# Kernel tuning notes

Hardware: AMD Instinct MI355X
Metric: run time of the kernel (lower is better)

The kernel has to match this reference:

```python
import jax, jax.numpy as jnp
import numpy as np

POOL = 4      # pool_size
SR = 2        # sampling_ratio (fixed; torchvision adaptive default approximated)
C_IN = 1024
C1, C2 = 256, 128
OUT_DIM = 2048


def setup_inputs() -> dict:
    key = jax.random.key(0)
    ks = jax.random.split(key, 10)
    B, C, H, W = 8, C_IN, 64, 64
    N = 64
    x = jax.random.normal(ks[0], (B, C, H, W), dtype=jnp.float32)
    # boxes in image pixel coords (image is H*16 = 1024 px)
    img = 1024.0
    x1 = jax.random.uniform(ks[1], (B, N), minval=0.0, maxval=img - 260.0)
    y1 = jax.random.uniform(ks[2], (B, N), minval=0.0, maxval=img - 260.0)
    bw = jax.random.uniform(ks[3], (B, N), minval=32.0, maxval=256.0)
    bh = jax.random.uniform(ks[4], (B, N), minval=32.0, maxval=256.0)
    boxes = jnp.stack([x1, y1, x1 + bw, y1 + bh], axis=-1)  # [B,N,4]
    scale = jnp.float32(1.0 / 16.0)
    # detector params
    w1 = jax.random.normal(ks[5], (C1, C_IN), dtype=jnp.float32) / np.sqrt(C_IN)
    b1 = jnp.zeros((C1,), dtype=jnp.float32)
    w2 = jax.random.normal(ks[6], (C2, C1), dtype=jnp.float32) / np.sqrt(C1)
    b2 = jnp.zeros((C2,), dtype=jnp.float32)
    wl = jax.random.normal(ks[7], (OUT_DIM, C2 * POOL * POOL), dtype=jnp.float32) / np.sqrt(C2 * POOL * POOL)
    bl = jnp.zeros((OUT_DIM,), dtype=jnp.float32)
    return {"x": x, "boxes": boxes, "scale": scale,
            "w1": w1, "b1": b1, "w2": w2, "b2": b2, "wl": wl, "bl": bl}


def _axis_coords(start, size, H):
    # start,size: [R]; returns coords [R, POOL*SR], valid mask, int low/high, lerp wts
    bin_sz = size / POOL                       # [R]
    j = jnp.arange(POOL * SR, dtype=jnp.float32)
    off = jnp.floor(j / SR) + ((j % SR) + 0.5) / SR   # [P]
    c = start[:, None] + off[None, :] * bin_sz[:, None]  # [R,P]
    valid = (c >= -1.0) & (c <= H)
    c = jnp.clip(c, 0.0, H - 1.0)
    lo = jnp.floor(c).astype(jnp.int32)
    lo = jnp.minimum(lo, H - 1)
    hi = jnp.minimum(lo + 1, H - 1)
    frac = c - lo.astype(c.dtype)
    return valid, lo, hi, frac


def _roi_align(feat, boxes, scale):
    # feat: [B,C,H,W], boxes: [B,N,4] -> pooled [B*N, C, POOL, POOL]
    B, C, H, W = feat.shape
    N = boxes.shape[1]
    R = B * N
    bx = (boxes.reshape(R, 4) * scale)
    x1, y1, x2, y2 = bx[:, 0], bx[:, 1], bx[:, 2], bx[:, 3]
    rw = jnp.maximum(x2 - x1, 1.0)
    rh = jnp.maximum(y2 - y1, 1.0)
    vy, y_lo, y_hi, ly = _axis_coords(y1, rh, H)   # [R,P]
    vx, x_lo, x_hi, lx = _axis_coords(x1, rw, W)
    hy, hx = 1.0 - ly, 1.0 - lx
    bidx = jnp.repeat(jnp.arange(B, dtype=jnp.int32), N)  # [R]
    b = bidx[:, None, None]
    # gather 4 corners -> [R,P,P,C]
    v00 = feat[b, :, y_lo[:, :, None], x_lo[:, None, :]]
    v01 = feat[b, :, y_lo[:, :, None], x_hi[:, None, :]]
    v10 = feat[b, :, y_hi[:, :, None], x_lo[:, None, :]]
    v11 = feat[b, :, y_hi[:, :, None], x_hi[:, None, :]]
    w00 = (hy[:, :, None] * hx[:, None, :])[..., None]
    w01 = (hy[:, :, None] * lx[:, None, :])[..., None]
    w10 = (ly[:, :, None] * hx[:, None, :])[..., None]
    w11 = (ly[:, :, None] * lx[:, None, :])[..., None]
    val = v00 * w00 + v01 * w01 + v10 * w10 + v11 * w11
    mask = (vy[:, :, None] & vx[:, None, :])[..., None]
    val = jnp.where(mask, val, 0.0)            # [R,P,P,C]
    val = val.reshape(R, POOL, SR, POOL, SR, C).mean(axis=(2, 4))  # [R,POOL,POOL,C]
    return jnp.transpose(val, (0, 3, 1, 2))    # [R,C,POOL,POOL]


def reference(x, boxes, scale, w1, b1, w2, b2, wl, bl):
    pooled = _roi_align(x, boxes, scale)                  # [R,C,4,4]
    h = jax.nn.elu(jnp.einsum('rchw,oc->rohw', pooled, w1) + b1[None, :, None, None])
    h = jax.nn.elu(jnp.einsum('rchw,oc->rohw', h, w2) + b2[None, :, None, None])
    h = h.reshape(h.shape[0], -1)                         # [R, 128*16], torch Flatten order
    out = jax.nn.elu(h @ wl.T + bl)                       # [R, 2048]
    return out
```

## Files before the change

### kernel.cpp

```cpp
#include <hip/hip_runtime.h>
#include <math.h>

#define C_INK   1024
#define C1D     256
#define C2D     128
#define OUTD    2048
#define R_ROI   512
#define MPIX    32768

#define NSIDE   128

typedef _Float16 half8 __attribute__((ext_vector_type(8)));
typedef float    f32x4 __attribute__((ext_vector_type(4)));

__device__ __forceinline__ unsigned int pack2h(float a, float b) {
    union { _Float16 h[2]; unsigned int u; } p;
    p.h[0] = (_Float16)a; p.h[1] = (_Float16)b;
    return p.u;
}
__device__ __forceinline__ float eluf(float v) { return v > 0.f ? v : expf(v) - 1.f; }

template<int RC>
__device__ __forceinline__ half8* ldsq(_Float16* base, int row, int ch) {
    return reinterpret_cast<half8*>(base) + row * RC + (ch ^ (row & 7));
}

__global__ __launch_bounds__(512, 4) void conv1x1_f16(
    const float* __restrict__ x, const float* __restrict__ w1,
    const float* __restrict__ w2, const float* __restrict__ wl,
    _Float16* __restrict__ w2h, _Float16* __restrict__ wlh,
    _Float16* __restrict__ z)
{
    const int bid = blockIdx.x;
    const int tid = threadIdx.x;

    if (bid < NSIDE) {
        constexpr int NF4_W2 = (C2D * C1D) / 4;
        constexpr int NF4    = NF4_W2 + (OUTD * OUTD) / 4;
        for (int i = bid * 512 + tid; i < NF4; i += NSIDE * 512) {
            const float* s; _Float16* d; int e;
            if (i < NF4_W2) { s = w2; d = w2h; e = i * 4; }
            else            { s = wl; d = wlh; e = (i - NF4_W2) * 4; }
            const float4 v = *reinterpret_cast<const float4*>(s + e);
            uint2 u; u.x = pack2h(v.x, v.y); u.y = pack2h(v.z, v.w);
            *reinterpret_cast<uint2*>(d + e) = u;
        }
        return;
    }

    __shared__ __align__(16) _Float16 As[64 * 64];
    __shared__ __align__(16) _Float16 Bs[256 * 64];

    const int lane = tid & 63;
    const int wave = tid >> 6;
    const int m0   = (bid - NSIDE) * 64;
    const int b    = m0 >> 12;
    const int p0   = m0 & 4095;

    const int bc  = tid & 7;
    const int br0 = tid >> 3;

    float ar[8];
    half8 brg[4];
    f32x4 acc[4][2];
    #pragma unroll
    for (int i = 0; i < 4; ++i)
        #pragma unroll
        for (int j = 0; j < 2; ++j) acc[i][j] = (f32x4){0.f, 0.f, 0.f, 0.f};

    const float* xbase = x + (size_t)b * C_INK * 4096 + p0 + lane;

    auto LOADT = [&](int k0) {
        const float* xk = xbase + (size_t)(k0 + wave * 8) * 4096;
        #pragma unroll
        for (int j = 0; j < 8; ++j) ar[j] = xk[(size_t)j * 4096];
        #pragma unroll
        for (int i = 0; i < 4; ++i) {
            const float* wp = &w1[(size_t)(br0 + i * 64) * C_INK + k0 + bc * 8];
            const float4 v0 = *reinterpret_cast<const float4*>(wp);
            const float4 v1 = *reinterpret_cast<const float4*>(wp + 4);
            union { half8 h; unsigned int u[4]; } pk;
            pk.u[0] = pack2h(v0.x, v0.y); pk.u[1] = pack2h(v0.z, v0.w);
            pk.u[2] = pack2h(v1.x, v1.y); pk.u[3] = pack2h(v1.z, v1.w);
            brg[i] = pk.h;
        }
    };
    auto WRITET = [&]() {
        union { half8 h; unsigned int u[4]; } pk;
        #pragma unroll
        for (int j = 0; j < 4; ++j) pk.u[j] = pack2h(ar[2 * j], ar[2 * j + 1]);
        *ldsq<8>(As, lane, wave) = pk.h;
        #pragma unroll
        for (int i = 0; i < 4; ++i) *ldsq<8>(Bs, br0 + i * 64, bc) = brg[i];
    };
    auto COMPUTET = [&]() {
        #pragma unroll
        for (int kk = 0; kk < 2; ++kk) {
            const int ch = kk * 4 + (lane >> 4);
            half8 af[4], bf[2];
            #pragma unroll
            for (int mi = 0; mi < 4; ++mi) af[mi] = *ldsq<8>(As, mi * 16 + (lane & 15), ch);
            #pragma unroll
            for (int ni = 0; ni < 2; ++ni) bf[ni] = *ldsq<8>(Bs, wave * 32 + ni * 16 + (lane & 15), ch);
            #pragma unroll
            for (int mi = 0; mi < 4; ++mi)
                #pragma unroll
                for (int ni = 0; ni < 2; ++ni)
                    acc[mi][ni] = __builtin_amdgcn_mfma_f32_16x16x32_f16(bf[ni], af[mi], acc[mi][ni], 0, 0, 0);
        }
    };

    LOADT(0); WRITET(); __syncthreads();
    for (int t = 0; t < 15; ++t) {
        LOADT((t + 1) * 64);
        COMPUTET();
        __syncthreads();
        WRITET();
        __syncthreads();
    }
    COMPUTET();

    _Float16* zp = z + (size_t)m0 * C1D;
    #pragma unroll
    for (int mi = 0; mi < 4; ++mi) {
        const int pixel = mi * 16 + (lane & 15);
        #pragma unroll
        for (int ni = 0; ni < 2; ++ni) {
            const int oc0 = wave * 32 + ni * 16 + (lane >> 4) * 4;
            uint2 u;
            u.x = pack2h(acc[mi][ni][0], acc[mi][ni][1]);
            u.y = pack2h(acc[mi][ni][2], acc[mi][ni][3]);
            *reinterpret_cast<uint2*>(&zp[(size_t)pixel * C1D + oc0]) = u;
        }
    }
}

__global__ __launch_bounds__(512) void roi_gemm2_f16(
    const _Float16* __restrict__ z, const float* __restrict__ boxes,
    const float* __restrict__ scale_p, const float* __restrict__ b1v,
    const _Float16* __restrict__ w2h, const float* __restrict__ b2v,
    _Float16* __restrict__ h2)
{
    __shared__ __align__(16) _Float16 H1s[16 * 256];
    __shared__ int   s_off[64][4];
    __shared__ float s_w[64][4];

    const int bid  = blockIdx.x;
    const int r    = (bid & 7) * 64 + (bid >> 3);
    const int tid  = threadIdx.x;
    const int lane = tid & 63;
    const int wv   = tid >> 6;

    half8 bfr[8];
    {
        const _Float16* wp = w2h + (size_t)(wv * 16 + (lane & 15)) * C1D + (lane >> 4) * 8;
        #pragma unroll
        for (int ks = 0; ks < 8; ++ks)
            bfr[ks] = *reinterpret_cast<const half8*>(wp + ks * 32);
    }

    if (tid < 64) {
        const float sc = scale_p[0];
        const float x1 = boxes[r * 4 + 0] * sc, y1 = boxes[r * 4 + 1] * sc;
        const float x2 = boxes[r * 4 + 2] * sc, y2 = boxes[r * 4 + 3] * sc;
        const float rw = fmaxf(x2 - x1, 1.f), rh = fmaxf(y2 - y1, 1.f);
        const int jy = tid >> 3, jx = tid & 7;

        float offy = (float)(jy >> 1) + (float)(jy & 1) * 0.5f + 0.25f;
        float cy = y1 + offy * rh * 0.25f;
        const bool vy = (cy >= -1.f) && (cy <= 64.f);
        cy = fminf(fmaxf(cy, 0.f), 63.f);
        int ylo = (int)cy; if (ylo > 63) ylo = 63;
        int yhi = ylo + 1; if (yhi > 63) yhi = 63;
        const float ly = cy - (float)ylo, hy = 1.f - ly;

        float offx = (float)(jx >> 1) + (float)(jx & 1) * 0.5f + 0.25f;
        float cx = x1 + offx * rw * 0.25f;
        const bool vx = (cx >= -1.f) && (cx <= 64.f);
        cx = fminf(fmaxf(cx, 0.f), 63.f);
        int xlo = (int)cx; if (xlo > 63) xlo = 63;
        int xhi = xlo + 1; if (xhi > 63) xhi = 63;
        const float lx = cx - (float)xlo, hx = 1.f - lx;

        const float wm = (vy && vx) ? 0.25f : 0.f;
        s_w[tid][0] = hy * hx * wm;
        s_w[tid][1] = hy * lx * wm;
        s_w[tid][2] = ly * hx * wm;
        s_w[tid][3] = ly * lx * wm;
        s_off[tid][0] = (ylo * 64 + xlo) * C1D;
        s_off[tid][1] = (ylo * 64 + xhi) * C1D;
        s_off[tid][2] = (yhi * 64 + xlo) * C1D;
        s_off[tid][3] = (yhi * 64 + xhi) * C1D;
    }
    __syncthreads();

    {
        const int ch8  = tid & 31;
        const int cell = tid >> 5;
        const _Float16* zb = z + (size_t)(r >> 6) * 4096 * C1D + ch8 * 8;

        float accv[8];
        #pragma unroll
        for (int e = 0; e < 8; ++e) accv[e] = 0.f;

        const int py = cell >> 2, px = cell & 3;
        #pragma unroll
        for (int u = 0; u < 4; ++u) {
            const int s = (py * 2 + (u >> 1)) * 8 + px * 2 + (u & 1);
            #pragma unroll
            for (int k = 0; k < 4; ++k) {
                const half8 v = *reinterpret_cast<const half8*>(zb + s_off[s][k]);
                const float w = s_w[s][k];
                #pragma unroll
                for (int e = 0; e < 8; ++e) accv[e] += (float)v[e] * w;
            }
        }

        const float4 b0 = *reinterpret_cast<const float4*>(&b1v[ch8 * 8]);
        const float4 b4 = *reinterpret_cast<const float4*>(&b1v[ch8 * 8 + 4]);
        half8 o;
        o[0] = (_Float16)eluf(accv[0] + b0.x); o[1] = (_Float16)eluf(accv[1] + b0.y);
        o[2] = (_Float16)eluf(accv[2] + b0.z); o[3] = (_Float16)eluf(accv[3] + b0.w);
        o[4] = (_Float16)eluf(accv[4] + b4.x); o[5] = (_Float16)eluf(accv[5] + b4.y);
        o[6] = (_Float16)eluf(accv[6] + b4.z); o[7] = (_Float16)eluf(accv[7] + b4.w);
        *ldsq<32>(H1s, cell, ch8) = o;
    }
    __syncthreads();

    f32x4 oa = (f32x4){0.f, 0.f, 0.f, 0.f};
    #pragma unroll
    for (int ks = 0; ks < 8; ++ks) {
        const int ch = ks * 4 + (lane >> 4);
        const half8 af = *ldsq<32>(H1s, lane & 15, ch);
        oa = __builtin_amdgcn_mfma_f32_16x16x32_f16(af, bfr[ks], oa, 0, 0, 0);
    }

    {
        const int o  = wv * 16 + (lane & 15);
        const int p0 = (lane >> 4) * 4;
        const float bv = b2v[o];
        uint2 u;
        u.x = pack2h(eluf(oa[0] + bv), eluf(oa[1] + bv));
        u.y = pack2h(eluf(oa[2] + bv), eluf(oa[3] + bv));
        *reinterpret_cast<uint2*>(&h2[(size_t)r * 2048 + o * 16 + p0]) = u;
    }
}

__global__ __launch_bounds__(512) void gemm_nt_out(
    const _Float16* __restrict__ A, const _Float16* __restrict__ W,
    const float* __restrict__ bias, float* __restrict__ Cout)
{
    constexpr int K = OUTD, N = OUTD;
    __shared__ __align__(16) _Float16 As[64 * 128];
    __shared__ __align__(16) _Float16 Bs[64 * 128];

    const int bid  = blockIdx.x;
    const int m0   = (bid >> 5) * 64;
    const int n0   = (bid & 31) * 64;

    const int tid  = threadIdx.x;
    const int lane = tid & 63;
    const int wave = tid >> 6;
    const int wr   = wave >> 2, wc = wave & 3;
    const int c    = tid & 7;
    const int r0   = tid >> 3;

    half8 arg[2], brg[2];
    f32x4 acc[2];
    acc[0] = (f32x4){0.f, 0.f, 0.f, 0.f};
    acc[1] = (f32x4){0.f, 0.f, 0.f, 0.f};

    auto LOADT = [&](int k0) {
        const _Float16* ap = &A[(size_t)(m0 + r0) * K + k0 + c * 16];
        arg[0] = *reinterpret_cast<const half8*>(ap);
        arg[1] = *reinterpret_cast<const half8*>(ap + 8);
        const _Float16* wp = &W[(size_t)(n0 + r0) * K + k0 + c * 16];
        brg[0] = *reinterpret_cast<const half8*>(wp);
        brg[1] = *reinterpret_cast<const half8*>(wp + 8);
    };
    auto WRITET = [&]() {
        *ldsq<16>(As, r0, 2 * c)     = arg[0];
        *ldsq<16>(As, r0, 2 * c + 1) = arg[1];
        *ldsq<16>(Bs, r0, 2 * c)     = brg[0];
        *ldsq<16>(Bs, r0, 2 * c + 1) = brg[1];
    };
    auto COMPUTET = [&]() {
        #pragma unroll
        for (int kk = 0; kk < 4; ++kk) {
            const int ch = kk * 4 + (lane >> 4);
            half8 af[2], bf;
            af[0] = *ldsq<16>(As, wr * 32 + (lane & 15), ch);
            af[1] = *ldsq<16>(As, wr * 32 + 16 + (lane & 15), ch);
            bf    = *ldsq<16>(Bs, wc * 16 + (lane & 15), ch);
            acc[0] = __builtin_amdgcn_mfma_f32_16x16x32_f16(bf, af[0], acc[0], 0, 0, 0);
            acc[1] = __builtin_amdgcn_mfma_f32_16x16x32_f16(bf, af[1], acc[1], 0, 0, 0);
        }
    };

    constexpr int nt = K / 128;
    LOADT(0); WRITET(); __syncthreads();
    for (int t = 0; t < nt - 1; ++t) {
        LOADT((t + 1) * 128);
        COMPUTET();
        __syncthreads();
        WRITET();
        __syncthreads();
    }
    COMPUTET();

    #pragma unroll
    for (int mi = 0; mi < 2; ++mi) {
        const int row  = m0 + wr * 32 + mi * 16 + (lane & 15);
        const int col0 = n0 + wc * 16 + (lane >> 4) * 4;
        const float4 bv = *reinterpret_cast<const float4*>(&bias[col0]);
        float4 o;
        o.x = eluf(acc[mi][0] + bv.x);
        o.y = eluf(acc[mi][1] + bv.y);
        o.z = eluf(acc[mi][2] + bv.z);
        o.w = eluf(acc[mi][3] + bv.w);
        *reinterpret_cast<float4*>(&Cout[(size_t)row * N + col0]) = o;
    }
}

extern "C" void kernel_launch(void* const* d_in, const int* in_sizes, int n_in,
                              void* d_out, int out_size, void* d_ws, size_t ws_size,
                              hipStream_t stream) {
    const float* x     = (const float*)d_in[0];
    const float* boxes = (const float*)d_in[1];
    const float* scale = (const float*)d_in[2];
    const float* w1    = (const float*)d_in[3];
    const float* b1    = (const float*)d_in[4];
    const float* w2    = (const float*)d_in[5];
    const float* b2    = (const float*)d_in[6];
    const float* wl    = (const float*)d_in[7];
    const float* bl    = (const float*)d_in[8];
    float* out = (float*)d_out;

    _Float16* z   = (_Float16*)d_ws;
    _Float16* h2  = z   + (size_t)MPIX * C1D;
    _Float16* w2h = h2  + (size_t)R_ROI * OUTD;
    _Float16* wlh = w2h + (size_t)C2D * C1D;

    conv1x1_f16<<<dim3(NSIDE + MPIX / 64), dim3(512), 0, stream>>>(
        x, w1, w2, wl, w2h, wlh, z);

    roi_gemm2_f16<<<dim3(R_ROI), dim3(512), 0, stream>>>(
        z, boxes, scale, b1, w2h, b2, h2);

    gemm_nt_out<<<dim3(256), dim3(512), 0, stream>>>(h2, wlh, bl, out);
}
```

Measured before the change: 77.90 us.

## Pre-convert w1 to fp16 and load B fragments directly from global with double-buffered A

Adds a small kernel that converts w1 to fp16 once, then the conv GEMM loads its weight fragments straight from global memory into registers instead of staging them through LDS. The A tile (activations) is double-buffered in LDS with register prefetch two tiles ahead, which halves the barriers per K-step and removes the 32KB B shared buffer, allowing more occupancy. The cost is an extra kernel launch and redundant per-wave global reads of weights, which rely on the cache.

```diff
diff --git a/kernel.cpp b/kernel.cpp
--- a/kernel.cpp
+++ b/kernel.cpp
@@ -25,8 +25,21 @@
     return reinterpret_cast<half8*>(base) + row * RC + (ch ^ (row & 7));
 }
 
+__global__ __launch_bounds__(256) void cvt_w1(
+    const float* __restrict__ w1, _Float16* __restrict__ w1h)
+{
+    const int i0 = (blockIdx.x * 256 + threadIdx.x) * 4;
+    #pragma unroll
+    for (int j = 0; j < 4; ++j) {
+        const int i = (i0 + j) * 4;
+        const float4 v = *reinterpret_cast<const float4*>(w1 + i);
+        uint2 u; u.x = pack2h(v.x, v.y); u.y = pack2h(v.z, v.w);
+        *reinterpret_cast<uint2*>(w1h + i) = u;
+    }
+}
+
 __global__ __launch_bounds__(512, 4) void conv1x1_f16(
-    const float* __restrict__ x, const float* __restrict__ w1,
+    const float* __restrict__ x, const _Float16* __restrict__ w1h,
     const float* __restrict__ w2, const float* __restrict__ wl,
     _Float16* __restrict__ w2h, _Float16* __restrict__ wlh,
     _Float16* __restrict__ z)
@@ -48,8 +61,7 @@
         return;
     }
 
-    __shared__ __align__(16) _Float16 As[64 * 64];
-    __shared__ __align__(16) _Float16 Bs[256 * 64];
+    __shared__ __align__(16) _Float16 As[2][64 * 64];
 
     const int lane = tid & 63;
     const int wave = tid >> 6;
@@ -57,68 +69,73 @@
     const int b    = m0 >> 12;
     const int p0   = m0 & 4095;
 
-    const int bc  = tid & 7;
-    const int br0 = tid >> 3;
-
-    float ar[8];
-    half8 brg[4];
+    const float* xbase = x + (size_t)b * C_INK * 4096 + p0 + lane;
+    const _Float16* wbase = w1h + (size_t)(wave * 32 + (lane & 15)) * C_INK + (lane >> 4) * 8;
+
+    float ar_a[8], ar_b[8];
+    half8 bf_a[2][2], bf_b[2][2];
     f32x4 acc[4][2];
     #pragma unroll
     for (int i = 0; i < 4; ++i)
         #pragma unroll
         for (int j = 0; j < 2; ++j) acc[i][j] = (f32x4){0.f, 0.f, 0.f, 0.f};
 
-    const float* xbase = x + (size_t)b * C_INK * 4096 + p0 + lane;
-
-    auto LOADT = [&](int k0) {
+    auto LOADA = [&](float (&ar)[8], int k0) {
         const float* xk = xbase + (size_t)(k0 + wave * 8) * 4096;
         #pragma unroll
         for (int j = 0; j < 8; ++j) ar[j] = xk[(size_t)j * 4096];
-        #pragma unroll
-        for (int i = 0; i < 4; ++i) {
-            const float* wp = &w1[(size_t)(br0 + i * 64) * C_INK + k0 + bc * 8];
-            const float4 v0 = *reinterpret_cast<const float4*>(wp);
-            const float4 v1 = *reinterpret_cast<const float4*>(wp + 4);
-            union { half8 h; unsigned int u[4]; } pk;
-            pk.u[0] = pack2h(v0.x, v0.y); pk.u[1] = pack2h(v0.z, v0.w);
-            pk.u[2] = pack2h(v1.x, v1.y); pk.u[3] = pack2h(v1.z, v1.w);
-            brg[i] = pk.h;
-        }
-    };
-    auto WRITET = [&]() {
+    };
+    auto LOADB = [&](half8 (&bf)[2][2], int k0) {
+        #pragma unroll
+        for (int kk = 0; kk < 2; ++kk)
+            #pragma unroll
+            for (int ni = 0; ni < 2; ++ni)
+                bf[kk][ni] = *reinterpret_cast<const half8*>(
+                    wbase + (size_t)ni * 16 * C_INK + k0 + kk * 32);
+    };
+    auto WRITEA = [&](int buf, float (&ar)[8]) {
         union { half8 h; unsigned int u[4]; } pk;
         #pragma unroll
         for (int j = 0; j < 4; ++j) pk.u[j] = pack2h(ar[2 * j], ar[2 * j + 1]);
-        *ldsq<8>(As, lane, wave) = pk.h;
-        #pragma unroll
-        for (int i = 0; i < 4; ++i) *ldsq<8>(Bs, br0 + i * 64, bc) = brg[i];
-    };
-    auto COMPUTET = [&]() {
+        *ldsq<8>(&As[buf][0], lane, wave) = pk.h;
+    };
+    auto COMPUTE = [&](int buf, half8 (&bf)[2][2]) {
         #pragma unroll
         for (int kk = 0; kk < 2; ++kk) {
             const int ch = kk * 4 + (lane >> 4);
-            half8 af[4], bf[2];
+            half8 af[4];
             #pragma unroll
-            for (int mi = 0; mi < 4; ++mi) af[mi] = *ldsq<8>(As, mi * 16 + (lane & 15), ch);
-            #pragma unroll
-            for (int ni = 0; ni < 2; ++ni) bf[ni] = *ldsq<8>(Bs, wave * 32 + ni * 16 + (lane & 15), ch);
+            for (int mi = 0; mi < 4; ++mi)
+                af[mi] = *ldsq<8>(&As[buf][0], mi * 16 + (lane & 15), ch);
             #pragma unroll
             for (int mi = 0; mi < 4; ++mi)
                 #pragma unroll
                 for (int ni = 0; ni < 2; ++ni)
-                    acc[mi][ni] = __builtin_amdgcn_mfma_f32_16x16x32_f16(bf[ni], af[mi], acc[mi][ni], 0, 0, 0);
-        }
-    };
-
-    LOADT(0); WRITET(); __syncthreads();
-    for (int t = 0; t < 15; ++t) {
-        LOADT((t + 1) * 64);
-        COMPUTET();
+                    acc[mi][ni] = __builtin_amdgcn_mfma_f32_16x16x32_f16(bf[kk][ni], af[mi], acc[mi][ni], 0, 0, 0);
+        }
+    };
+
+    LOADA(ar_a, 0);   LOADB(bf_a, 0);
+    LOADA(ar_b, 64);  LOADB(bf_b, 64);
+    WRITEA(0, ar_a);
+    __syncthreads();
+
+    #pragma unroll
+    for (int tp = 0; tp < 8; ++tp) {
+        const int t = 2 * tp;
+        if (tp < 7) LOADA(ar_a, (t + 2) * 64);
+        WRITEA(1, ar_b);
+        COMPUTE(0, bf_a);
+        if (tp < 7) LOADB(bf_a, (t + 2) * 64);
         __syncthreads();
-        WRITET();
+        if (tp < 7) {
+            LOADA(ar_b, (t + 3) * 64);
+            WRITEA(0, ar_a);
+        }
+        COMPUTE(1, bf_b);
+        if (tp < 7) LOADB(bf_b, (t + 3) * 64);
         __syncthreads();
     }
-    COMPUTET();
 
     _Float16* zp = z + (size_t)m0 * C1D;
     #pragma unroll
@@ -338,11 +355,14 @@
 
     _Float16* z   = (_Float16*)d_ws;
     _Float16* h2  = z   + (size_t)MPIX * C1D;
-    _Float16* w2h = h2  + (size_t)R_ROI * OUTD;
+    _Float16* w1h = h2  + (size_t)R_ROI * OUTD;
+    _Float16* w2h = w1h + (size_t)C1D * C_INK;
     _Float16* wlh = w2h + (size_t)C2D * C1D;
 
+    cvt_w1<<<dim3(64), dim3(256), 0, stream>>>(w1, w1h);
+
     conv1x1_f16<<<dim3(NSIDE + MPIX / 64), dim3(512), 0, stream>>>(
-        x, w1, w2, wl, w2h, wlh, z);
+        x, w1h, w2, wl, w2h, wlh, z);
 
     roi_gemm2_f16<<<dim3(R_ROI), dim3(512), 0, stream>>>(
         z, boxes, scale, b1, w2h, b2, h2);
```

Result: no change. 77.47 us (median of 6 runs) (-0.6%).
